# Optimization experiments

Hardware: AMD Instinct MI355X
Metric: run time of the kernel (lower is better)

## Reference

```python
import jax, jax.numpy as jnp
import numpy as np

N = 65536
DIMS = [512, 1000, 500, 250, 1]


def setup_inputs() -> dict:
    key = jax.random.key(0)
    ks = jax.random.split(key, 7)

    def init_w(k, fan_in, fan_out):
        return (jax.random.normal(k, (fan_in, fan_out), jnp.float32)
                / np.float32(np.sqrt(fan_in)))

    return {
        "repr_xy_hat": jax.random.normal(ks[0], (N, DIMS[0]), jnp.float32),
        "repr_xy": jax.random.normal(ks[1], (N, DIMS[0]), jnp.float32),
        "W1": init_w(ks[2], DIMS[0], DIMS[1]), "b1": jnp.zeros((DIMS[1],), jnp.float32),
        "W2": init_w(ks[3], DIMS[1], DIMS[2]), "b2": jnp.zeros((DIMS[2],), jnp.float32),
        "W3": init_w(ks[4], DIMS[2], DIMS[3]), "b3": jnp.zeros((DIMS[3],), jnp.float32),
        "W4": init_w(ks[5], DIMS[3], DIMS[4]), "b4": jnp.zeros((DIMS[4],), jnp.float32),
    }


def _disc_logits(x, W1, b1, W2, b2, W3, b3, W4, b4):
    # Batched version of the per-sample Linear-ReLU chain; sigmoid is folded
    # into the numerically stable BCE losses below.
    h = jax.nn.relu(x @ W1 + b1)
    h = jax.nn.relu(h @ W2 + b2)
    h = jax.nn.relu(h @ W3 + b3)
    return (h @ W4 + b4)[:, 0]  # [N]


def reference(repr_xy_hat, repr_xy, W1, b1, W2, b2, W3, b3, W4, b4):
    z_fake = _disc_logits(repr_xy_hat, W1, b1, W2, b2, W3, b3, W4, b4)  # [N]
    z_real = _disc_logits(repr_xy, W1, b1, W2, b2, W3, b3, W4, b4)      # [N]
    # generator loss: sum_i -log sigmoid(z_fake_i) = softplus(-z_fake)
    loss_F = jnp.sum(jax.nn.softplus(-z_fake))
    # discriminator loss: sum_i [-log sigmoid(z_real_i) - log(1 - sigmoid(z_fake_i))]
    # pred is detached in the original -> stop_gradient on the fake logits.
    z_fake_d = jax.lax.stop_gradient(z_fake)
    loss_D = jnp.sum(jax.nn.softplus(-z_real) + jax.nn.softplus(z_fake_d))
    return (loss_F, loss_D)
```

## Files before the change

### kernel.cpp

```cpp
#include <hip/hip_runtime.h>
#include <hip/hip_bf16.h>
#include <cmath>

using short4v = __attribute__((ext_vector_type(4))) short;
using f32x16  = __attribute__((ext_vector_type(16))) float;
using int8v   = __attribute__((ext_vector_type(8))) int;

#define MFMASC(a,b,c) __builtin_amdgcn_mfma_scale_f32_32x32x64_f8f6f4( \
    a, b, c, 0, 0, 0, 0x7F7F7F7F, 0, 0x7F7F7F7F)

__device__ __forceinline__ unsigned short f2bf(float f) {
    union { float f; unsigned u; } v; v.f = f;
    unsigned u = v.u;
    return (unsigned short)((u + 0x7FFFu + ((u >> 16) & 1u)) >> 16);
}
__device__ __forceinline__ float bf2f(unsigned short h) {
    union { unsigned u; float f; } v; v.u = ((unsigned)h) << 16;
    return v.f;
}
__device__ __forceinline__ float softplus(float x) {
    return fmaxf(x, 0.f) + log1pf(expf(-fabsf(x)));
}
__device__ __forceinline__ unsigned f4_to_fp8x4(float a, float b, float c, float d) {
    int v = __builtin_amdgcn_cvt_pk_fp8_f32(a, b, 0, false);
    v = __builtin_amdgcn_cvt_pk_fp8_f32(c, d, v, true);
    return (unsigned)v;
}
__device__ __forceinline__ int8v ld_a(const unsigned char* base, int o0, int o1) {
    int8v r;
    *((uint4*)&r)     = *(const uint4*)(base + o0);
    *((uint4*)&r + 1) = *(const uint4*)(base + o1);
    return r;
}
__device__ __forceinline__ int8v ld_w(const uint4* p) {
    int8v r;
    *((uint4*)&r)     = p[0];
    *((uint4*)&r + 1) = p[1];
    return r;
}

__device__ __forceinline__ void pack_one(const float* __restrict__ W,
                                         uint4* __restrict__ out,
                                         int K_real, int M_real, int KG, int tid) {
    int lane = tid & 63;
    int t    = tid >> 6;
    int kg   = t % KG;
    int ct   = t / KG;
    int m  = ct * 32 + (lane & 31);
    int kb = kg * 64 + ((lane >> 5) << 5);
    float f[32];
#pragma unroll
    for (int j = 0; j < 32; ++j) {
        int k = kb + j;
        f[j] = (k < K_real && m < M_real) ? W[(size_t)k * M_real + m] : 0.f;
    }
    uint4 o0, o1;
    o0.x = f4_to_fp8x4(f[0],  f[1],  f[2],  f[3]);
    o0.y = f4_to_fp8x4(f[4],  f[5],  f[6],  f[7]);
    o0.z = f4_to_fp8x4(f[8],  f[9],  f[10], f[11]);
    o0.w = f4_to_fp8x4(f[12], f[13], f[14], f[15]);
    o1.x = f4_to_fp8x4(f[16], f[17], f[18], f[19]);
    o1.y = f4_to_fp8x4(f[20], f[21], f[22], f[23]);
    o1.z = f4_to_fp8x4(f[24], f[25], f[26], f[27]);
    o1.w = f4_to_fp8x4(f[28], f[29], f[30], f[31]);
    out[(size_t)tid * 2]     = o0;
    out[(size_t)tid * 2 + 1] = o1;
}

__global__ void prep_all(const float* __restrict__ W1, const float* __restrict__ W2,
                         const float* __restrict__ W3, const float* __restrict__ b1,
                         const float* __restrict__ b2, const float* __restrict__ b3,
                         uint4* __restrict__ pW1, uint4* __restrict__ pW2,
                         uint4* __restrict__ pW3, float* __restrict__ biasp) {
    int tid = blockIdx.x * 256 + threadIdx.x;
    if (tid < 16384) {
        pack_one(W1, pW1, 512, 1000, 8, tid);
    } else if (tid < 32768) {
        pack_one(W2, pW2, 1000, 500, 16, tid - 16384);
    } else if (tid < 36864) {
        pack_one(W3, pW3, 500, 250, 8, tid - 32768);
    } else if (tid < 38656) {
        int i = tid - 36864;
        if (i < 1024)      biasp[i] = (i < 1000) ? b1[i] : 0.f;
        else if (i < 1536) { int j = i - 1024; biasp[i] = (j < 500) ? b2[j] : 0.f; }
        else               { int j = i - 1536; biasp[i] = (j < 250) ? b3[j] : 0.f; }
    }
}

__global__ __launch_bounds__(512, 4) void fused_mlp(
    const float* __restrict__ Xf, const float* __restrict__ Xr,
    const uint4* __restrict__ pW1, const uint4* __restrict__ pW2,
    const uint4* __restrict__ pW3, const float* __restrict__ biasp,
    const float* __restrict__ W4, const float* __restrict__ b4,
    float* __restrict__ partials)
{
    __shared__ __align__(16) unsigned char smem[66048];
    float* red = (float*)(smem + 65536);

    const int tidx = threadIdx.x;
    const int wid  = tidx >> 6;
    const int lane = tidx & 63;
    const int l31  = lane & 31;
    const int hi   = lane >> 5;
    const int swz  = (l31 & 15) << 4;

    const long grow0 = (long)blockIdx.x * 64;
    const float* X = (grow0 < 65536) ? (Xf + (size_t)grow0 * 512)
                                     : (Xr + (size_t)(grow0 - 65536) * 512);

#pragma unroll 1
    for (int gb = 0; gb < 4; ++gb) {
        float4 xr[4];
#pragma unroll
        for (int it = 0; it < 4; ++it) {
            int idx = (gb * 4 + it) * 512 + tidx;
            int r = idx >> 7; int k0 = (idx & 127) * 4;
            xr[it] = *(const float4*)(X + (size_t)r * 512 + k0);
        }
#pragma unroll
        for (int it = 0; it < 4; ++it) {
            int idx = (gb * 4 + it) * 512 + tidx;
            int r = idx >> 7; int k0 = (idx & 127) * 4;
            int pos = 512 + ((k0 & 0x1F0) ^ ((r & 15) << 4)) + (k0 & 12);
            *(unsigned*)(smem + r * 1024 + pos) =
                f4_to_fp8x4(xr[it].x, xr[it].y, xr[it].z, xr[it].w);
        }
    }
    __syncthreads();

#pragma unroll 1
    for (int p = 0; p < 2; ++p) {
        const uint4* wpA = pW1 + ((size_t)((p * 16 + wid * 2 + 0) * 8) * 64 + lane) * 2;
        const uint4* wpB = pW1 + ((size_t)((p * 16 + wid * 2 + 1) * 8) * 64 + lane) * 2;
        f32x16 acc[2][2];
#pragma unroll
        for (int c = 0; c < 2; ++c)
#pragma unroll
            for (int rt = 0; rt < 2; ++rt)
#pragma unroll
                for (int g = 0; g < 16; ++g) acc[c][rt][g] = 0.f;

#pragma unroll 1
        for (int kg = 0; kg < 8; ++kg) {
            int k0 = kg * 64 + hi * 32;
            const unsigned char* r0 = smem + l31 * 1024 + 512;
            const unsigned char* r1 = smem + (32 + l31) * 1024 + 512;
            int8v a0 = ld_a(r0, k0 ^ swz, (k0 + 16) ^ swz);
            int8v a1 = ld_a(r1, k0 ^ swz, (k0 + 16) ^ swz);
            int8v w0 = ld_w(wpA + (size_t)kg * 128);
            int8v w1 = ld_w(wpB + (size_t)kg * 128);
            __builtin_amdgcn_s_setprio(1);
            acc[0][0] = MFMASC(w0, a0, acc[0][0]);
            acc[0][1] = MFMASC(w0, a1, acc[0][1]);
            acc[1][0] = MFMASC(w1, a0, acc[1][0]);
            acc[1][1] = MFMASC(w1, a1, acc[1][1]);
            __builtin_amdgcn_s_setprio(0);
        }
        if (p == 1) __syncthreads();
#pragma unroll
        for (int c = 0; c < 2; ++c) {
            int mt = (p * 16 + wid * 2 + c) * 32;
#pragma unroll
            for (int rt = 0; rt < 2; ++rt) {
                int row = rt * 32 + l31;
#pragma unroll
                for (int q = 0; q < 4; ++q) {
                    int mg = mt + q * 8 + hi * 4;
                    float4 bb = *(const float4*)(biasp + mg);
                    float v0 = fmaxf(acc[c][rt][q * 4 + 0] + bb.x, 0.f);
                    float v1 = fmaxf(acc[c][rt][q * 4 + 1] + bb.y, 0.f);
                    float v2 = fmaxf(acc[c][rt][q * 4 + 2] + bb.z, 0.f);
                    float v3 = fmaxf(acc[c][rt][q * 4 + 3] + bb.w, 0.f);
                    *(unsigned*)(smem + row * 1024 + (mg ^ swz)) =
                        f4_to_fp8x4(v0, v1, v2, v3);
                }
            }
        }
    }
    __syncthreads();

    {
        const uint4* wpA = pW2 + ((size_t)((wid * 2 + 0) * 16) * 64 + lane) * 2;
        const uint4* wpB = pW2 + ((size_t)((wid * 2 + 1) * 16) * 64 + lane) * 2;
        f32x16 acc[2][2];
#pragma unroll
        for (int c = 0; c < 2; ++c)
#pragma unroll
            for (int rt = 0; rt < 2; ++rt)
#pragma unroll
                for (int g = 0; g < 16; ++g) acc[c][rt][g] = 0.f;
#pragma unroll 1
        for (int kg = 0; kg < 16; ++kg) {
            int k0 = kg * 64 + hi * 32;
            const unsigned char* r0 = smem + l31 * 1024;
            const unsigned char* r1 = smem + (32 + l31) * 1024;
            int8v a0 = ld_a(r0, k0 ^ swz, (k0 + 16) ^ swz);
            int8v a1 = ld_a(r1, k0 ^ swz, (k0 + 16) ^ swz);
            int8v w0 = ld_w(wpA + (size_t)kg * 128);
            int8v w1 = ld_w(wpB + (size_t)kg * 128);
            __builtin_amdgcn_s_setprio(1);
            acc[0][0] = MFMASC(w0, a0, acc[0][0]);
            acc[0][1] = MFMASC(w0, a1, acc[0][1]);
            acc[1][0] = MFMASC(w1, a0, acc[1][0]);
            acc[1][1] = MFMASC(w1, a1, acc[1][1]);
            __builtin_amdgcn_s_setprio(0);
        }
        __syncthreads();
#pragma unroll
        for (int c = 0; c < 2; ++c) {
            int mt = (wid * 2 + c) * 32;
#pragma unroll
            for (int rt = 0; rt < 2; ++rt) {
                int row = rt * 32 + l31;
#pragma unroll
                for (int q = 0; q < 4; ++q) {
                    int mg = mt + q * 8 + hi * 4;
                    float4 bb = *(const float4*)(biasp + 1024 + mg);
                    float v0 = fmaxf(acc[c][rt][q * 4 + 0] + bb.x, 0.f);
                    float v1 = fmaxf(acc[c][rt][q * 4 + 1] + bb.y, 0.f);
                    float v2 = fmaxf(acc[c][rt][q * 4 + 2] + bb.z, 0.f);
                    float v3 = fmaxf(acc[c][rt][q * 4 + 3] + bb.w, 0.f);
                    *(unsigned*)(smem + row * 512 + (mg ^ swz)) =
                        f4_to_fp8x4(v0, v1, v2, v3);
                }
            }
        }
    }
    __syncthreads();

    {
        const uint4* wp = pW3 + ((size_t)(wid * 8) * 64 + lane) * 2;
        f32x16 acc3[2];
#pragma unroll
        for (int rt = 0; rt < 2; ++rt)
#pragma unroll
            for (int g = 0; g < 16; ++g) acc3[rt][g] = 0.f;
#pragma unroll 1
        for (int kg = 0; kg < 8; ++kg) {
            int k0 = kg * 64 + hi * 32;
            const unsigned char* r0 = smem + l31 * 512;
            const unsigned char* r1 = smem + (32 + l31) * 512;
            int8v a0 = ld_a(r0, k0 ^ swz, (k0 + 16) ^ swz);
            int8v a1 = ld_a(r1, k0 ^ swz, (k0 + 16) ^ swz);
            int8v w = ld_w(wp + (size_t)kg * 128);
            __builtin_amdgcn_s_setprio(1);
            acc3[0] = MFMASC(w, a0, acc3[0]);
            acc3[1] = MFMASC(w, a1, acc3[1]);
            __builtin_amdgcn_s_setprio(0);
        }
        int mt = wid * 32;
#pragma unroll
        for (int rt = 0; rt < 2; ++rt) {
            int row = rt * 32 + l31;
#pragma unroll
            for (int q = 0; q < 4; ++q) {
                int mg = mt + q * 8 + hi * 4;
                float4 bb = *(const float4*)(biasp + 1536 + mg);
                short4v s;
                s[0] = (short)f2bf(fmaxf(acc3[rt][q * 4 + 0] + bb.x, 0.f));
                s[1] = (short)f2bf(fmaxf(acc3[rt][q * 4 + 1] + bb.y, 0.f));
                s[2] = (short)f2bf(fmaxf(acc3[rt][q * 4 + 2] + bb.z, 0.f));
                s[3] = (short)f2bf(fmaxf(acc3[rt][q * 4 + 3] + bb.w, 0.f));
                *(short4v*)(smem + 32768 + row * 512 + ((mg * 2) ^ swz)) = s;
            }
        }
    }
    __syncthreads();

    {
        int g  = tidx >> 3;
        int t8 = tidx & 7;
        int gs = (g & 15) << 4;
        float sum = 0.f;
#pragma unroll
        for (int o = 0; o < 4; ++o) {
            int colb = t8 * 32 + o * 8;
            short4v v0 = *(const short4v*)(smem + 32768 + g * 512 + ((colb * 2) ^ gs));
            short4v v1 = *(const short4v*)(smem + 32768 + g * 512 + ((colb * 2 + 8) ^ gs));
#pragma unroll
            for (int j = 0; j < 4; ++j) {
                int c0 = colb + j, c1 = colb + 4 + j;
                if (c0 < 250) sum += bf2f((unsigned short)v0[j]) * W4[c0];
                if (c1 < 250) sum += bf2f((unsigned short)v1[j]) * W4[c1];
            }
        }
        sum += __shfl_down(sum, 4, 8);
        sum += __shfl_down(sum, 2, 8);
        sum += __shfl_down(sum, 1, 8);
        if (t8 == 0) {
            float z = sum + b4[0];
            bool fake = (grow0 < 65536);
            float spn = softplus(-z);
            red[g]      = fake ? spn : 0.f;
            red[64 + g] = fake ? softplus(z) : spn;
        }
    }
    __syncthreads();
    if (tidx == 0) {
        float pF = 0.f, pD = 0.f;
        for (int i = 0; i < 64; ++i) { pF += red[i]; pD += red[64 + i]; }
        partials[(size_t)blockIdx.x * 2]     = pF;
        partials[(size_t)blockIdx.x * 2 + 1] = pD;
    }
}

__global__ void reduce_partials(const float* __restrict__ partials, int nblocks,
                                float* __restrict__ out) {
    __shared__ float sF[256], sD[256];
    float f = 0.f, d = 0.f;
    for (int i = threadIdx.x; i < nblocks; i += 256) {
        f += partials[2 * i];
        d += partials[2 * i + 1];
    }
    sF[threadIdx.x] = f; sD[threadIdx.x] = d;
    __syncthreads();
    for (int s = 128; s > 0; s >>= 1) {
        if (threadIdx.x < s) {
            sF[threadIdx.x] += sF[threadIdx.x + s];
            sD[threadIdx.x] += sD[threadIdx.x + s];
        }
        __syncthreads();
    }
    if (threadIdx.x == 0) { out[0] = sF[0]; out[1] = sD[0]; }
}

extern "C" void kernel_launch(void* const* d_in, const int* in_sizes, int n_in,
                              void* d_out, int out_size, void* d_ws, size_t ws_size,
                              hipStream_t stream) {
    const float* Xf = (const float*)d_in[0];
    const float* Xr = (const float*)d_in[1];
    const float* W1 = (const float*)d_in[2];
    const float* b1 = (const float*)d_in[3];
    const float* W2 = (const float*)d_in[4];
    const float* b2 = (const float*)d_in[5];
    const float* W3 = (const float*)d_in[6];
    const float* b3 = (const float*)d_in[7];
    const float* W4 = (const float*)d_in[8];
    const float* b4 = (const float*)d_in[9];

    uint4* pW1 = (uint4*)d_ws;
    uint4* pW2 = pW1 + 32768;
    uint4* pW3 = pW2 + 32768;
    float* biasp = (float*)(pW3 + 8192);
    float* partials = biasp + 2048;

    prep_all<<<151, 256, 0, stream>>>(W1, W2, W3, b1, b2, b3,
                                      pW1, pW2, pW3, biasp);

    fused_mlp<<<2048, 512, 0, stream>>>(Xf, Xr, pW1, pW2, pW3,
                                        biasp, W4, b4, partials);

    reduce_partials<<<1, 256, 0, stream>>>(partials, 2048, (float*)d_out);
}
```

Before: 186.8 us.

## Halve block to 256 threads, doubling output tiles per wave in each layer

The fused MLP block shrinks from 8 to 4 waves. Each wave now computes four 32-column weight tiles per layer instead of two (two instead of one in layer 3), so each loaded activation fragment feeds more MFMAs. The input load loop and the final dot-product reduction are rescaled to match. This trades more accumulator registers per wave and fewer waves per CU (launch bounds 256,2) for less LDS activation reloading per MFMA.

```diff
diff --git a/kernel.cpp b/kernel.cpp
--- a/kernel.cpp
+++ b/kernel.cpp
@@ -87,7 +87,7 @@
     }
 }
 
-__global__ __launch_bounds__(512, 4) void fused_mlp(
+__global__ __launch_bounds__(256, 2) void fused_mlp(
     const float* __restrict__ Xf, const float* __restrict__ Xr,
     const uint4* __restrict__ pW1, const uint4* __restrict__ pW2,
     const uint4* __restrict__ pW3, const float* __restrict__ biasp,
@@ -109,17 +109,17 @@
                                      : (Xr + (size_t)(grow0 - 65536) * 512);
 
 #pragma unroll 1
-    for (int gb = 0; gb < 4; ++gb) {
+    for (int gb = 0; gb < 8; ++gb) {
         float4 xr[4];
 #pragma unroll
         for (int it = 0; it < 4; ++it) {
-            int idx = (gb * 4 + it) * 512 + tidx;
+            int idx = (gb * 4 + it) * 256 + tidx;
             int r = idx >> 7; int k0 = (idx & 127) * 4;
             xr[it] = *(const float4*)(X + (size_t)r * 512 + k0);
         }
 #pragma unroll
         for (int it = 0; it < 4; ++it) {
-            int idx = (gb * 4 + it) * 512 + tidx;
+            int idx = (gb * 4 + it) * 256 + tidx;
             int r = idx >> 7; int k0 = (idx & 127) * 4;
             int pos = 512 + ((k0 & 0x1F0) ^ ((r & 15) << 4)) + (k0 & 12);
             *(unsigned*)(smem + r * 1024 + pos) =
@@ -130,11 +130,13 @@
 
 #pragma unroll 1
     for (int p = 0; p < 2; ++p) {
-        const uint4* wpA = pW1 + ((size_t)((p * 16 + wid * 2 + 0) * 8) * 64 + lane) * 2;
-        const uint4* wpB = pW1 + ((size_t)((p * 16 + wid * 2 + 1) * 8) * 64 + lane) * 2;
-        f32x16 acc[2][2];
-#pragma unroll
-        for (int c = 0; c < 2; ++c)
+        const uint4* wp0 = pW1 + ((size_t)((p * 16 + wid * 4 + 0) * 8) * 64 + lane) * 2;
+        const uint4* wp1 = pW1 + ((size_t)((p * 16 + wid * 4 + 1) * 8) * 64 + lane) * 2;
+        const uint4* wp2 = pW1 + ((size_t)((p * 16 + wid * 4 + 2) * 8) * 64 + lane) * 2;
+        const uint4* wp3 = pW1 + ((size_t)((p * 16 + wid * 4 + 3) * 8) * 64 + lane) * 2;
+        f32x16 acc[4][2];
+#pragma unroll
+        for (int c = 0; c < 4; ++c)
 #pragma unroll
             for (int rt = 0; rt < 2; ++rt)
 #pragma unroll
@@ -147,19 +149,25 @@
             const unsigned char* r1 = smem + (32 + l31) * 1024 + 512;
             int8v a0 = ld_a(r0, k0 ^ swz, (k0 + 16) ^ swz);
             int8v a1 = ld_a(r1, k0 ^ swz, (k0 + 16) ^ swz);
-            int8v w0 = ld_w(wpA + (size_t)kg * 128);
-            int8v w1 = ld_w(wpB + (size_t)kg * 128);
+            int8v w0 = ld_w(wp0 + (size_t)kg * 128);
+            int8v w1 = ld_w(wp1 + (size_t)kg * 128);
+            int8v w2 = ld_w(wp2 + (size_t)kg * 128);
+            int8v w3 = ld_w(wp3 + (size_t)kg * 128);
             __builtin_amdgcn_s_setprio(1);
             acc[0][0] = MFMASC(w0, a0, acc[0][0]);
             acc[0][1] = MFMASC(w0, a1, acc[0][1]);
             acc[1][0] = MFMASC(w1, a0, acc[1][0]);
             acc[1][1] = MFMASC(w1, a1, acc[1][1]);
+            acc[2][0] = MFMASC(w2, a0, acc[2][0]);
+            acc[2][1] = MFMASC(w2, a1, acc[2][1]);
+            acc[3][0] = MFMASC(w3, a0, acc[3][0]);
+            acc[3][1] = MFMASC(w3, a1, acc[3][1]);
             __builtin_amdgcn_s_setprio(0);
         }
         if (p == 1) __syncthreads();
 #pragma unroll
-        for (int c = 0; c < 2; ++c) {
-            int mt = (p * 16 + wid * 2 + c) * 32;
+        for (int c = 0; c < 4; ++c) {
+            int mt = (p * 16 + wid * 4 + c) * 32;
 #pragma unroll
             for (int rt = 0; rt < 2; ++rt) {
                 int row = rt * 32 + l31;
@@ -180,11 +188,13 @@
     __syncthreads();
 
     {
-        const uint4* wpA = pW2 + ((size_t)((wid * 2 + 0) * 16) * 64 + lane) * 2;
-        const uint4* wpB = pW2 + ((size_t)((wid * 2 + 1) * 16) * 64 + lane) * 2;
-        f32x16 acc[2][2];
-#pragma unroll
-        for (int c = 0; c < 2; ++c)
+        const uint4* wp0 = pW2 + ((size_t)((wid * 4 + 0) * 16) * 64 + lane) * 2;
+        const uint4* wp1 = pW2 + ((size_t)((wid * 4 + 1) * 16) * 64 + lane) * 2;
+        const uint4* wp2 = pW2 + ((size_t)((wid * 4 + 2) * 16) * 64 + lane) * 2;
+        const uint4* wp3 = pW2 + ((size_t)((wid * 4 + 3) * 16) * 64 + lane) * 2;
+        f32x16 acc[4][2];
+#pragma unroll
+        for (int c = 0; c < 4; ++c)
 #pragma unroll
             for (int rt = 0; rt < 2; ++rt)
 #pragma unroll
@@ -196,19 +206,25 @@
             const unsigned char* r1 = smem + (32 + l31) * 1024;
             int8v a0 = ld_a(r0, k0 ^ swz, (k0 + 16) ^ swz);
             int8v a1 = ld_a(r1, k0 ^ swz, (k0 + 16) ^ swz);
-            int8v w0 = ld_w(wpA + (size_t)kg * 128);
-            int8v w1 = ld_w(wpB + (size_t)kg * 128);
+            int8v w0 = ld_w(wp0 + (size_t)kg * 128);
+            int8v w1 = ld_w(wp1 + (size_t)kg * 128);
+            int8v w2 = ld_w(wp2 + (size_t)kg * 128);
+            int8v w3 = ld_w(wp3 + (size_t)kg * 128);
             __builtin_amdgcn_s_setprio(1);
             acc[0][0] = MFMASC(w0, a0, acc[0][0]);
             acc[0][1] = MFMASC(w0, a1, acc[0][1]);
             acc[1][0] = MFMASC(w1, a0, acc[1][0]);
             acc[1][1] = MFMASC(w1, a1, acc[1][1]);
+            acc[2][0] = MFMASC(w2, a0, acc[2][0]);
+            acc[2][1] = MFMASC(w2, a1, acc[2][1]);
+            acc[3][0] = MFMASC(w3, a0, acc[3][0]);
+            acc[3][1] = MFMASC(w3, a1, acc[3][1]);
             __builtin_amdgcn_s_setprio(0);
         }
         __syncthreads();
 #pragma unroll
-        for (int c = 0; c < 2; ++c) {
-            int mt = (wid * 2 + c) * 32;
+        for (int c = 0; c < 4; ++c) {
+            int mt = (wid * 4 + c) * 32;
 #pragma unroll
             for (int rt = 0; rt < 2; ++rt) {
                 int row = rt * 32 + l31;
@@ -229,12 +245,15 @@
     __syncthreads();
 
     {
-        const uint4* wp = pW3 + ((size_t)(wid * 8) * 64 + lane) * 2;
-        f32x16 acc3[2];
-#pragma unroll
-        for (int rt = 0; rt < 2; ++rt)
-#pragma unroll
-            for (int g = 0; g < 16; ++g) acc3[rt][g] = 0.f;
+        const uint4* wp0 = pW3 + ((size_t)((wid * 2 + 0) * 8) * 64 + lane) * 2;
+        const uint4* wp1 = pW3 + ((size_t)((wid * 2 + 1) * 8) * 64 + lane) * 2;
+        f32x16 acc3[2][2];
+#pragma unroll
+        for (int c = 0; c < 2; ++c)
+#pragma unroll
+            for (int rt = 0; rt < 2; ++rt)
+#pragma unroll
+                for (int g = 0; g < 16; ++g) acc3[c][rt][g] = 0.f;
 #pragma unroll 1
         for (int kg = 0; kg < 8; ++kg) {
             int k0 = kg * 64 + hi * 32;
@@ -242,39 +261,45 @@
             const unsigned char* r1 = smem + (32 + l31) * 512;
             int8v a0 = ld_a(r0, k0 ^ swz, (k0 + 16) ^ swz);
             int8v a1 = ld_a(r1, k0 ^ swz, (k0 + 16) ^ swz);
-            int8v w = ld_w(wp + (size_t)kg * 128);
+            int8v w0 = ld_w(wp0 + (size_t)kg * 128);
+            int8v w1 = ld_w(wp1 + (size_t)kg * 128);
             __builtin_amdgcn_s_setprio(1);
-            acc3[0] = MFMASC(w, a0, acc3[0]);
-            acc3[1] = MFMASC(w, a1, acc3[1]);
+            acc3[0][0] = MFMASC(w0, a0, acc3[0][0]);
+            acc3[0][1] = MFMASC(w0, a1, acc3[0][1]);
+            acc3[1][0] = MFMASC(w1, a0, acc3[1][0]);
+            acc3[1][1] = MFMASC(w1, a1, acc3[1][1]);
             __builtin_amdgcn_s_setprio(0);
         }
-        int mt = wid * 32;
-#pragma unroll
-        for (int rt = 0; rt < 2; ++rt) {
-            int row = rt * 32 + l31;
-#pragma unroll
-            for (int q = 0; q < 4; ++q) {
-                int mg = mt + q * 8 + hi * 4;
-                float4 bb = *(const float4*)(biasp + 1536 + mg);
-                short4v s;
-                s[0] = (short)f2bf(fmaxf(acc3[rt][q * 4 + 0] + bb.x, 0.f));
-                s[1] = (short)f2bf(fmaxf(acc3[rt][q * 4 + 1] + bb.y, 0.f));
-                s[2] = (short)f2bf(fmaxf(acc3[rt][q * 4 + 2] + bb.z, 0.f));
-                s[3] = (short)f2bf(fmaxf(acc3[rt][q * 4 + 3] + bb.w, 0.f));
-                *(short4v*)(smem + 32768 + row * 512 + ((mg * 2) ^ swz)) = s;
+#pragma unroll
+        for (int c = 0; c < 2; ++c) {
+            int mt = (wid * 2 + c) * 32;
+#pragma unroll
+            for (int rt = 0; rt < 2; ++rt) {
+                int row = rt * 32 + l31;
+#pragma unroll
+                for (int q = 0; q < 4; ++q) {
+                    int mg = mt + q * 8 + hi * 4;
+                    float4 bb = *(const float4*)(biasp + 1536 + mg);
+                    short4v s;
+                    s[0] = (short)f2bf(fmaxf(acc3[c][rt][q * 4 + 0] + bb.x, 0.f));
+                    s[1] = (short)f2bf(fmaxf(acc3[c][rt][q * 4 + 1] + bb.y, 0.f));
+                    s[2] = (short)f2bf(fmaxf(acc3[c][rt][q * 4 + 2] + bb.z, 0.f));
+                    s[3] = (short)f2bf(fmaxf(acc3[c][rt][q * 4 + 3] + bb.w, 0.f));
+                    *(short4v*)(smem + 32768 + row * 512 + ((mg * 2) ^ swz)) = s;
+                }
             }
         }
     }
     __syncthreads();
 
     {
-        int g  = tidx >> 3;
-        int t8 = tidx & 7;
+        int g  = tidx >> 2;
+        int t4 = tidx & 3;
         int gs = (g & 15) << 4;
         float sum = 0.f;
 #pragma unroll
-        for (int o = 0; o < 4; ++o) {
-            int colb = t8 * 32 + o * 8;
+        for (int o = 0; o < 8; ++o) {
+            int colb = t4 * 64 + o * 8;
             short4v v0 = *(const short4v*)(smem + 32768 + g * 512 + ((colb * 2) ^ gs));
             short4v v1 = *(const short4v*)(smem + 32768 + g * 512 + ((colb * 2 + 8) ^ gs));
 #pragma unroll
@@ -284,10 +309,9 @@
                 if (c1 < 250) sum += bf2f((unsigned short)v1[j]) * W4[c1];
             }
         }
-        sum += __shfl_down(sum, 4, 8);
-        sum += __shfl_down(sum, 2, 8);
-        sum += __shfl_down(sum, 1, 8);
-        if (t8 == 0) {
+        sum += __shfl_down(sum, 2, 4);
+        sum += __shfl_down(sum, 1, 4);
+        if (t4 == 0) {
             float z = sum + b4[0];
             bool fake = (grow0 < 65536);
             float spn = softplus(-z);
@@ -347,7 +371,7 @@
     prep_all<<<151, 256, 0, stream>>>(W1, W2, W3, b1, b2, b3,
                                       pW1, pW2, pW3, biasp);
 
-    fused_mlp<<<2048, 512, 0, stream>>>(Xf, Xr, pW1, pW2, pW3,
+    fused_mlp<<<2048, 256, 0, stream>>>(Xf, Xr, pW1, pW2, pW3,
                                         biasp, W4, b4, partials);
 
     reduce_partials<<<1, 256, 0, stream>>>(partials, 2048, (float*)d_out);
```

After: 182.5 us, median of 2. 2.3% less time.

## Double rows per block to 128 to improve weight reuse per MFMA

Applied to the files above, without the earlier changes.

Each block now processes 128 rows instead of 64. Every loaded weight fragment feeds four row-tile MFMAs instead of two, which halves global weight traffic per row and the grid size. The price is twice the LDS (about 129 KB) and twice the accumulator registers. Launch bounds drop to one block per CU, so occupancy and latency hiding fall.

```diff
diff --git a/kernel.cpp b/kernel.cpp
--- a/kernel.cpp
+++ b/kernel.cpp
@@ -87,15 +87,15 @@
     }
 }
 
-__global__ __launch_bounds__(512, 4) void fused_mlp(
+__global__ __launch_bounds__(512, 1) void fused_mlp(
     const float* __restrict__ Xf, const float* __restrict__ Xr,
     const uint4* __restrict__ pW1, const uint4* __restrict__ pW2,
     const uint4* __restrict__ pW3, const float* __restrict__ biasp,
     const float* __restrict__ W4, const float* __restrict__ b4,
     float* __restrict__ partials)
 {
-    __shared__ __align__(16) unsigned char smem[66048];
-    float* red = (float*)(smem + 65536);
+    __shared__ __align__(16) unsigned char smem[132096];
+    float* red = (float*)(smem + 131072);
 
     const int tidx = threadIdx.x;
     const int wid  = tidx >> 6;
@@ -104,12 +104,12 @@
     const int hi   = lane >> 5;
     const int swz  = (l31 & 15) << 4;
 
-    const long grow0 = (long)blockIdx.x * 64;
+    const long grow0 = (long)blockIdx.x * 128;
     const float* X = (grow0 < 65536) ? (Xf + (size_t)grow0 * 512)
                                      : (Xr + (size_t)(grow0 - 65536) * 512);
 
 #pragma unroll 1
-    for (int gb = 0; gb < 4; ++gb) {
+    for (int gb = 0; gb < 8; ++gb) {
         float4 xr[4];
 #pragma unroll
         for (int it = 0; it < 4; ++it) {
@@ -130,30 +130,34 @@
 
 #pragma unroll 1
     for (int p = 0; p < 2; ++p) {
-        const uint4* wpA = pW1 + ((size_t)((p * 16 + wid * 2 + 0) * 8) * 64 + lane) * 2;
-        const uint4* wpB = pW1 + ((size_t)((p * 16 + wid * 2 + 1) * 8) * 64 + lane) * 2;
-        f32x16 acc[2][2];
+        const uint4* wp0 = pW1 + ((size_t)((p * 16 + wid * 2 + 0) * 8) * 64 + lane) * 2;
+        const uint4* wp1 = pW1 + ((size_t)((p * 16 + wid * 2 + 1) * 8) * 64 + lane) * 2;
+        f32x16 acc[2][4];
 #pragma unroll
         for (int c = 0; c < 2; ++c)
 #pragma unroll
-            for (int rt = 0; rt < 2; ++rt)
+            for (int rt = 0; rt < 4; ++rt)
 #pragma unroll
                 for (int g = 0; g < 16; ++g) acc[c][rt][g] = 0.f;
 
 #pragma unroll 1
         for (int kg = 0; kg < 8; ++kg) {
             int k0 = kg * 64 + hi * 32;
-            const unsigned char* r0 = smem + l31 * 1024 + 512;
-            const unsigned char* r1 = smem + (32 + l31) * 1024 + 512;
-            int8v a0 = ld_a(r0, k0 ^ swz, (k0 + 16) ^ swz);
-            int8v a1 = ld_a(r1, k0 ^ swz, (k0 + 16) ^ swz);
-            int8v w0 = ld_w(wpA + (size_t)kg * 128);
-            int8v w1 = ld_w(wpB + (size_t)kg * 128);
+            int8v a0 = ld_a(smem + (0 * 32 + l31) * 1024 + 512, k0 ^ swz, (k0 + 16) ^ swz);
+            int8v a1 = ld_a(smem + (1 * 32 + l31) * 1024 + 512, k0 ^ swz, (k0 + 16) ^ swz);
+            int8v a2 = ld_a(smem + (2 * 32 + l31) * 1024 + 512, k0 ^ swz, (k0 + 16) ^ swz);
+            int8v a3 = ld_a(smem + (3 * 32 + l31) * 1024 + 512, k0 ^ swz, (k0 + 16) ^ swz);
+            int8v w0 = ld_w(wp0 + (size_t)kg * 128);
+            int8v w1 = ld_w(wp1 + (size_t)kg * 128);
             __builtin_amdgcn_s_setprio(1);
             acc[0][0] = MFMASC(w0, a0, acc[0][0]);
             acc[0][1] = MFMASC(w0, a1, acc[0][1]);
+            acc[0][2] = MFMASC(w0, a2, acc[0][2]);
+            acc[0][3] = MFMASC(w0, a3, acc[0][3]);
             acc[1][0] = MFMASC(w1, a0, acc[1][0]);
             acc[1][1] = MFMASC(w1, a1, acc[1][1]);
+            acc[1][2] = MFMASC(w1, a2, acc[1][2]);
+            acc[1][3] = MFMASC(w1, a3, acc[1][3]);
             __builtin_amdgcn_s_setprio(0);
         }
         if (p == 1) __syncthreads();
@@ -161,7 +165,7 @@
         for (int c = 0; c < 2; ++c) {
             int mt = (p * 16 + wid * 2 + c) * 32;
 #pragma unroll
-            for (int rt = 0; rt < 2; ++rt) {
+            for (int rt = 0; rt < 4; ++rt) {
                 int row = rt * 32 + l31;
 #pragma unroll
                 for (int q = 0; q < 4; ++q) {
@@ -180,29 +184,33 @@
     __syncthreads();
 
     {
-        const uint4* wpA = pW2 + ((size_t)((wid * 2 + 0) * 16) * 64 + lane) * 2;
-        const uint4* wpB = pW2 + ((size_t)((wid * 2 + 1) * 16) * 64 + lane) * 2;
-        f32x16 acc[2][2];
+        const uint4* wp0 = pW2 + ((size_t)((wid * 2 + 0) * 16) * 64 + lane) * 2;
+        const uint4* wp1 = pW2 + ((size_t)((wid * 2 + 1) * 16) * 64 + lane) * 2;
+        f32x16 acc[2][4];
 #pragma unroll
         for (int c = 0; c < 2; ++c)
 #pragma unroll
-            for (int rt = 0; rt < 2; ++rt)
+            for (int rt = 0; rt < 4; ++rt)
 #pragma unroll
                 for (int g = 0; g < 16; ++g) acc[c][rt][g] = 0.f;
 #pragma unroll 1
         for (int kg = 0; kg < 16; ++kg) {
             int k0 = kg * 64 + hi * 32;
-            const unsigned char* r0 = smem + l31 * 1024;
-            const unsigned char* r1 = smem + (32 + l31) * 1024;
-            int8v a0 = ld_a(r0, k0 ^ swz, (k0 + 16) ^ swz);
-            int8v a1 = ld_a(r1, k0 ^ swz, (k0 + 16) ^ swz);
-            int8v w0 = ld_w(wpA + (size_t)kg * 128);
-            int8v w1 = ld_w(wpB + (size_t)kg * 128);
+            int8v a0 = ld_a(smem + (0 * 32 + l31) * 1024, k0 ^ swz, (k0 + 16) ^ swz);
+            int8v a1 = ld_a(smem + (1 * 32 + l31) * 1024, k0 ^ swz, (k0 + 16) ^ swz);
+            int8v a2 = ld_a(smem + (2 * 32 + l31) * 1024, k0 ^ swz, (k0 + 16) ^ swz);
+            int8v a3 = ld_a(smem + (3 * 32 + l31) * 1024, k0 ^ swz, (k0 + 16) ^ swz);
+            int8v w0 = ld_w(wp0 + (size_t)kg * 128);
+            int8v w1 = ld_w(wp1 + (size_t)kg * 128);
             __builtin_amdgcn_s_setprio(1);
             acc[0][0] = MFMASC(w0, a0, acc[0][0]);
             acc[0][1] = MFMASC(w0, a1, acc[0][1]);
+            acc[0][2] = MFMASC(w0, a2, acc[0][2]);
+            acc[0][3] = MFMASC(w0, a3, acc[0][3]);
             acc[1][0] = MFMASC(w1, a0, acc[1][0]);
             acc[1][1] = MFMASC(w1, a1, acc[1][1]);
+            acc[1][2] = MFMASC(w1, a2, acc[1][2]);
+            acc[1][3] = MFMASC(w1, a3, acc[1][3]);
             __builtin_amdgcn_s_setprio(0);
         }
         __syncthreads();
@@ -210,7 +218,7 @@
         for (int c = 0; c < 2; ++c) {
             int mt = (wid * 2 + c) * 32;
 #pragma unroll
-            for (int rt = 0; rt < 2; ++rt) {
+            for (int rt = 0; rt < 4; ++rt) {
                 int row = rt * 32 + l31;
 #pragma unroll
                 for (int q = 0; q < 4; ++q) {
@@ -230,27 +238,29 @@
 
     {
         const uint4* wp = pW3 + ((size_t)(wid * 8) * 64 + lane) * 2;
-        f32x16 acc3[2];
-#pragma unroll
-        for (int rt = 0; rt < 2; ++rt)
+        f32x16 acc3[4];
+#pragma unroll
+        for (int rt = 0; rt < 4; ++rt)
 #pragma unroll
             for (int g = 0; g < 16; ++g) acc3[rt][g] = 0.f;
 #pragma unroll 1
         for (int kg = 0; kg < 8; ++kg) {
             int k0 = kg * 64 + hi * 32;
-            const unsigned char* r0 = smem + l31 * 512;
-            const unsigned char* r1 = smem + (32 + l31) * 512;
-            int8v a0 = ld_a(r0, k0 ^ swz, (k0 + 16) ^ swz);
-            int8v a1 = ld_a(r1, k0 ^ swz, (k0 + 16) ^ swz);
+            int8v a0 = ld_a(smem + (0 * 32 + l31) * 512, k0 ^ swz, (k0 + 16) ^ swz);
+            int8v a1 = ld_a(smem + (1 * 32 + l31) * 512, k0 ^ swz, (k0 + 16) ^ swz);
+            int8v a2 = ld_a(smem + (2 * 32 + l31) * 512, k0 ^ swz, (k0 + 16) ^ swz);
+            int8v a3 = ld_a(smem + (3 * 32 + l31) * 512, k0 ^ swz, (k0 + 16) ^ swz);
             int8v w = ld_w(wp + (size_t)kg * 128);
             __builtin_amdgcn_s_setprio(1);
             acc3[0] = MFMASC(w, a0, acc3[0]);
             acc3[1] = MFMASC(w, a1, acc3[1]);
+            acc3[2] = MFMASC(w, a2, acc3[2]);
+            acc3[3] = MFMASC(w, a3, acc3[3]);
             __builtin_amdgcn_s_setprio(0);
         }
         int mt = wid * 32;
 #pragma unroll
-        for (int rt = 0; rt < 2; ++rt) {
+        for (int rt = 0; rt < 4; ++rt) {
             int row = rt * 32 + l31;
 #pragma unroll
             for (int q = 0; q < 4; ++q) {
@@ -261,22 +271,22 @@
                 s[1] = (short)f2bf(fmaxf(acc3[rt][q * 4 + 1] + bb.y, 0.f));
                 s[2] = (short)f2bf(fmaxf(acc3[rt][q * 4 + 2] + bb.z, 0.f));
                 s[3] = (short)f2bf(fmaxf(acc3[rt][q * 4 + 3] + bb.w, 0.f));
-                *(short4v*)(smem + 32768 + row * 512 + ((mg * 2) ^ swz)) = s;
+                *(short4v*)(smem + 65536 + row * 512 + ((mg * 2) ^ swz)) = s;
             }
         }
     }
     __syncthreads();
 
     {
-        int g  = tidx >> 3;
-        int t8 = tidx & 7;
+        int g  = tidx >> 2;
+        int t4 = tidx & 3;
         int gs = (g & 15) << 4;
         float sum = 0.f;
 #pragma unroll
-        for (int o = 0; o < 4; ++o) {
-            int colb = t8 * 32 + o * 8;
-            short4v v0 = *(const short4v*)(smem + 32768 + g * 512 + ((colb * 2) ^ gs));
-            short4v v1 = *(const short4v*)(smem + 32768 + g * 512 + ((colb * 2 + 8) ^ gs));
+        for (int o = 0; o < 8; ++o) {
+            int colb = t4 * 64 + o * 8;
+            short4v v0 = *(const short4v*)(smem + 65536 + g * 512 + ((colb * 2) ^ gs));
+            short4v v1 = *(const short4v*)(smem + 65536 + g * 512 + ((colb * 2 + 8) ^ gs));
 #pragma unroll
             for (int j = 0; j < 4; ++j) {
                 int c0 = colb + j, c1 = colb + 4 + j;
@@ -284,21 +294,20 @@
                 if (c1 < 250) sum += bf2f((unsigned short)v1[j]) * W4[c1];
             }
         }
-        sum += __shfl_down(sum, 4, 8);
-        sum += __shfl_down(sum, 2, 8);
-        sum += __shfl_down(sum, 1, 8);
-        if (t8 == 0) {
+        sum += __shfl_down(sum, 2, 4);
+        sum += __shfl_down(sum, 1, 4);
+        if (t4 == 0) {
             float z = sum + b4[0];
             bool fake = (grow0 < 65536);
             float spn = softplus(-z);
-            red[g]      = fake ? spn : 0.f;
-            red[64 + g] = fake ? softplus(z) : spn;
+            red[g]       = fake ? spn : 0.f;
+            red[128 + g] = fake ? softplus(z) : spn;
         }
     }
     __syncthreads();
     if (tidx == 0) {
         float pF = 0.f, pD = 0.f;
-        for (int i = 0; i < 64; ++i) { pF += red[i]; pD += red[64 + i]; }
+        for (int i = 0; i < 128; ++i) { pF += red[i]; pD += red[128 + i]; }
         partials[(size_t)blockIdx.x * 2]     = pF;
         partials[(size_t)blockIdx.x * 2 + 1] = pD;
     }
@@ -347,8 +356,8 @@
     prep_all<<<151, 256, 0, stream>>>(W1, W2, W3, b1, b2, b3,
                                       pW1, pW2, pW3, biasp);
 
-    fused_mlp<<<2048, 512, 0, stream>>>(Xf, Xr, pW1, pW2, pW3,
+    fused_mlp<<<1024, 512, 0, stream>>>(Xf, Xr, pW1, pW2, pW3,
                                         biasp, W4, b4, partials);
 
-    reduce_partials<<<1, 256, 0, stream>>>(partials, 2048, (float*)d_out);
-}
+    reduce_partials<<<1, 256, 0, stream>>>(partials, 1024, (float*)d_out);
+}
```

New measurement: 194.5 us. 4.1% more time.
